# Optimization experiments

Hardware: AMD Instinct MI355X
Metric: run time of the kernel (lower is better)

Reference implementation:

```python
import jax, jax.numpy as jnp
import numpy as np

IN_FEATURES = 11008
OUT_FEATURES = 4096
TOPK = 5504            # in_features * topk_ratio (0.5)
RECALL_THRES = 0.9
N_CACHE = 64           # modeled steady-state cache size


def setup_inputs() -> dict:
    key = jax.random.key(0)
    k1, k2, k3, k4 = jax.random.split(key, 4)
    x = jax.random.normal(k1, (1, 1, IN_FEATURES), dtype=jnp.float32)
    weight = jax.random.normal(k2, (OUT_FEATURES, IN_FEATURES), dtype=jnp.float32) * 0.02
    bias = jax.random.normal(k3, (OUT_FEATURES,), dtype=jnp.float32) * 0.02
    cached_indices = jax.random.randint(k4, (N_CACHE, TOPK), 0, IN_FEATURES, dtype=jnp.int64)
    return {"x": x, "weight": weight, "bias": bias, "cached_indices": cached_indices}


def reference(x, weight, bias, cached_indices):
    # decode path: bsz == seq == 1
    xf = x.reshape(-1, IN_FEATURES)                       # [1, in]
    x_mean = jnp.abs(xf).mean(axis=0)                     # [in]
    # top-k neuron selection (argsort descending -> top_k)
    _, topk_idx = jax.lax.top_k(x_mean, TOPK)             # [topk]
    topk_mask = jnp.zeros((IN_FEATURES,), dtype=bool).at[topk_idx].set(True)
    # rebuild cached boolean masks from cached index sets
    cached_masks = (
        jnp.zeros((N_CACHE, IN_FEATURES), dtype=bool)
        .at[jnp.arange(N_CACHE)[:, None], cached_indices]
        .set(True)
    )
    # recall of each cached mask against current top-k mask
    intersection = jnp.sum(cached_masks & topk_mask[None, :], axis=1)  # [n_cache]
    recalls = intersection.astype(jnp.float32) / TOPK
    best_idx = jnp.argmax(recalls)
    best_recall = recalls[best_idx]
    # cache hit -> reuse cached indices; miss -> use fresh top-k indices
    idx = jnp.where(best_recall >= RECALL_THRES, cached_indices[best_idx], topk_idx)
    # gather sparse column slice, then small GEMM + bias
    w_slice = weight[:, idx]                               # [out, topk]
    out = xf[:, idx] @ w_slice.T + bias                    # [1, out]
    return out.reshape(1, 1, OUT_FEATURES)
```

## Files before the change

kernel.cpp:

```cpp
#include <hip/hip_runtime.h>
#include <stdint.h>

#define IN_F   11008
#define OUT_F  4096
#define TOPK_K 5504
#define NCACHE 64
#define MASK_WORDS 344
#define NCHUNK 11


__device__ __forceinline__ unsigned absbits(float v) {
    return __float_as_uint(v) & 0x7fffffffu;
}

__global__ __launch_bounds__(1024) void k_select(const float* __restrict__ x,
                                                 unsigned* __restrict__ maskbits_g,
                                                 unsigned* __restrict__ score_g) {
    __shared__ unsigned hist[16][256];
    __shared__ unsigned csum[256];
    __shared__ unsigned sh_T, sh_rem, sh_totEq;
    __shared__ unsigned waveEq[NCHUNK][16];
    __shared__ unsigned waveEqPre[NCHUNK][16];

    const int tid  = threadIdx.x;
    const int wv   = tid >> 6;
    const int lane = tid & 63;
    const int nk   = (tid < IN_F - 10 * 1024) ? NCHUNK : NCHUNK - 1;

    unsigned key[NCHUNK];
#pragma unroll
    for (int c = 0; c < NCHUNK; ++c) {
        key[c] = 0u;
        if (c < nk) key[c] = absbits(x[c * 1024 + tid]);
    }

    if (tid == 0) *score_g = 0;

    unsigned prefix = 0, maskHi = 0, remaining = TOPK_K;

    for (int pass = 3; pass >= 0; --pass) {
        const int sh = pass * 8;
        for (int b = tid; b < 16 * 256; b += 1024) ((unsigned*)hist)[b] = 0;
        __syncthreads();
#pragma unroll
        for (int c = 0; c < NCHUNK; ++c) {
            if (c < nk && (key[c] & maskHi) == prefix)
                atomicAdd(&hist[wv][(key[c] >> sh) & 255], 1u);
        }
        __syncthreads();
        if (tid < 256) {
            unsigned s = 0;
#pragma unroll
            for (int w = 0; w < 16; ++w) s += hist[w][tid];
            csum[tid] = s;
        }
        __syncthreads();
        if (wv == 0) {
            unsigned c0 = csum[4 * lane + 0], c1 = csum[4 * lane + 1];
            unsigned c2 = csum[4 * lane + 2], c3 = csum[4 * lane + 3];
            unsigned S = c0 + c1 + c2 + c3;
#pragma unroll
            for (int off = 1; off < 64; off <<= 1) {
                unsigned v = __shfl_down(S, off, 64);
                if (lane + off < 64) S += v;
            }
            unsigned Sn = __shfl_down(S, 1, 64);
            if (lane == 63) Sn = 0;
            unsigned t3 = Sn + c3;
            unsigned t2 = t3 + c2;
            unsigned t1 = t2 + c1;
            unsigned t0 = t1 + c0;
            unsigned rem = remaining;
            if (t3 >= rem && Sn < rem) { sh_T = prefix | ((unsigned)(4 * lane + 3) << sh); sh_rem = rem - Sn; }
            if (t2 >= rem && t3 < rem) { sh_T = prefix | ((unsigned)(4 * lane + 2) << sh); sh_rem = rem - t3; }
            if (t1 >= rem && t2 < rem) { sh_T = prefix | ((unsigned)(4 * lane + 1) << sh); sh_rem = rem - t2; }
            if (t0 >= rem && t1 < rem) { sh_T = prefix | ((unsigned)(4 * lane + 0) << sh); sh_rem = rem - t1; }
        }
        __syncthreads();
        prefix = sh_T;
        maskHi |= 0xffu << sh;
        remaining = sh_rem;
    }

    const unsigned T = prefix;
    const unsigned eqTake = remaining;

    unsigned gtm = 0, eqm = 0;
#pragma unroll
    for (int c = 0; c < NCHUNK; ++c) {
        if (c < nk) {
            if (key[c] > T)       gtm |= 1u << c;
            else if (key[c] == T) eqm |= 1u << c;
        }
    }
#pragma unroll
    for (int c = 0; c < NCHUNK; ++c) {
        unsigned long long bal = __ballot((eqm >> c) & 1u);
        if (lane == 0) waveEq[c][wv] = (unsigned)__popcll(bal);
    }
    __syncthreads();
    if (tid < 64) {
        unsigned s = 0;
        for (int p = lane; p < NCHUNK * 16; p += 64) s += waveEq[p >> 4][p & 15];
#pragma unroll
        for (int off = 32; off > 0; off >>= 1) s += __shfl_down(s, off, 64);
        if (lane == 0) sh_totEq = s;
    }
    __syncthreads();
    const bool fast = (sh_totEq == eqTake);
    if (!fast) {
        if (tid == 0) {
            unsigned run = 0;
            for (int c = 0; c < NCHUNK; ++c)
                for (int w = 0; w < 16; ++w) { waveEqPre[c][w] = run; run += waveEq[c][w]; }
        }
        __syncthreads();
    }
#pragma unroll
    for (int c = 0; c < NCHUNK; ++c) {
        bool eq = (eqm >> c) & 1u;
        bool take;
        if (fast) {
            take = (((gtm >> c) & 1u) != 0u) || eq;
        } else {
            unsigned long long balEq = __ballot(eq);
            unsigned rank = waveEqPre[c][wv] + (unsigned)__popcll(balEq & ((1ull << lane) - 1ull));
            take = (((gtm >> c) & 1u) != 0u) || (eq && rank < eqTake);
        }
        unsigned long long balT = __ballot(take);
        int w0 = c * 32 + wv * 2;
        if (w0 < MASK_WORDS && lane == 0) {
            maskbits_g[w0]     = (unsigned)balT;
            maskbits_g[w0 + 1] = (unsigned)(balT >> 32);
        }
    }
}

__global__ __launch_bounds__(256) void k_recall(const int* __restrict__ cached,
                                                const unsigned* __restrict__ maskbits_g,
                                                unsigned* __restrict__ score_g) {
    __shared__ unsigned rowbits[MASK_WORDS];
    __shared__ unsigned wsum[4];
    const int r = blockIdx.x;
    const int tid = threadIdx.x;
    for (int w = tid; w < MASK_WORDS; w += 256) rowbits[w] = 0;
    __syncthreads();
    const int4* ci4 = (const int4*)(cached + (size_t)r * TOPK_K);
    for (int t = tid; t < TOPK_K / 4; t += 256) {
        int4 v = ci4[t];
        atomicOr(&rowbits[v.x >> 5], 1u << (v.x & 31));
        atomicOr(&rowbits[v.y >> 5], 1u << (v.y & 31));
        atomicOr(&rowbits[v.z >> 5], 1u << (v.z & 31));
        atomicOr(&rowbits[v.w >> 5], 1u << (v.w & 31));
    }
    __syncthreads();
    unsigned cnt = 0;
    for (int w = tid; w < MASK_WORDS; w += 256) cnt += __popc(rowbits[w] & maskbits_g[w]);
    for (int off = 32; off > 0; off >>= 1) cnt += __shfl_down(cnt, off, 64);
    if ((tid & 63) == 0) wsum[tid >> 6] = cnt;
    __syncthreads();
    if (tid == 0) {
        unsigned tot = wsum[0] + wsum[1] + wsum[2] + wsum[3];
        atomicMax(score_g, (tot << 6) | (unsigned)(63 - r));
    }
}

#define ROWS_PER_BLOCK 16
#define GEMV_THREADS   512
__global__ __launch_bounds__(GEMV_THREADS) void k_gemv(const float* __restrict__ x,
                                                       const float* __restrict__ W,
                                                       const float* __restrict__ bias,
                                                       const unsigned* __restrict__ maskbits_g,
                                                       const unsigned* __restrict__ score_g,
                                                       const int* __restrict__ cached,
                                                       float* __restrict__ out) {
    __shared__ __align__(16) float xs[IN_F];
    const int tid = threadIdx.x;

    unsigned score = *score_g;
    unsigned inter = score >> 6;
    bool useCache = ((float)inter / (float)TOPK_K) >= 0.9f;

    if (useCache) {
        int best = 63 - (int)(score & 63u);
        for (int i = tid; i < IN_F; i += GEMV_THREADS) xs[i] = 0.f;
        __syncthreads();
        const int* ci = cached + (size_t)best * TOPK_K;
        for (int t = tid; t < TOPK_K; t += GEMV_THREADS) {
            int idx = ci[t];
            atomicAdd(&xs[idx], x[idx]);
        }
    } else {
        const float4* x4 = (const float4*)x;
        for (int j = tid; j < IN_F / 4; j += GEMV_THREADS) {
            float4 xv = x4[j];
            int base = j * 4;
            unsigned wbits = maskbits_g[base >> 5];
            int sh = base & 31;
            xs[base + 0] = xv.x * (float)((wbits >> (sh + 0)) & 1u);
            xs[base + 1] = xv.y * (float)((wbits >> (sh + 1)) & 1u);
            xs[base + 2] = xv.z * (float)((wbits >> (sh + 2)) & 1u);
            xs[base + 3] = xv.w * (float)((wbits >> (sh + 3)) & 1u);
        }
    }
    __syncthreads();

    const int wv   = tid >> 6;
    const int lane = tid & 63;
    const int row0 = blockIdx.x * ROWS_PER_BLOCK + wv * 2;
    const int row1 = row0 + 1;
    const float4* w0p = (const float4*)(W + (size_t)row0 * IN_F);
    const float4* w1p = (const float4*)(W + (size_t)row1 * IN_F);
    const float4* xs4 = (const float4*)xs;

    float acc0 = 0.f, acc1 = 0.f;
#pragma unroll 4
    for (int j = lane; j < IN_F / 4; j += 64) {
        float4 xv = xs4[j];
        float4 a  = w0p[j];
        float4 b  = w1p[j];
        acc0 += xv.x * a.x + xv.y * a.y + xv.z * a.z + xv.w * a.w;
        acc1 += xv.x * b.x + xv.y * b.y + xv.z * b.z + xv.w * b.w;
    }
    for (int off = 32; off > 0; off >>= 1) {
        acc0 += __shfl_down(acc0, off, 64);
        acc1 += __shfl_down(acc1, off, 64);
    }
    if (lane == 0) {
        out[row0] = acc0 + bias[row0];
        out[row1] = acc1 + bias[row1];
    }
}

extern "C" void kernel_launch(void* const* d_in, const int* in_sizes, int n_in,
                              void* d_out, int out_size, void* d_ws, size_t ws_size,
                              hipStream_t stream) {
    const float* x      = (const float*)d_in[0];
    const float* W      = (const float*)d_in[1];
    const float* bias   = (const float*)d_in[2];
    const int*   cached = (const int*)d_in[3];
    float* out = (float*)d_out;

    char* ws = (char*)d_ws;
    unsigned* maskbits = (unsigned*)(ws + 0);
    unsigned* score    = (unsigned*)(ws + 1408);

    k_select<<<1, 1024, 0, stream>>>(x, maskbits, score);
    k_recall<<<NCACHE, 256, 0, stream>>>(cached, maskbits, score);
    k_gemv<<<OUT_F / ROWS_PER_BLOCK, GEMV_THREADS, 0, stream>>>(x, W, bias, maskbits, score, cached, out);
}
```

Measured before the change: 280.1 us.

## Fuse select, recall and GEMV into one cooperative kernel with speculative GEMV

Merges the three launches into a single cooperative kernel of 256 blocks of 1024 threads, synchronised with grid.sync. While block 0 runs the top-k radix select, the other blocks touch their weight rows to warm the cache until a flag is raised. Each block then computes the GEMV speculatively with the fresh top-k mask while recall is still being evaluated. It redoes the GEMV with the cached index set only if the best recall passes the threshold. This removes launch gaps and overlaps selection with weight traffic, at the cost of two grid-wide barriers, a recompute on cache hits, and a single resident block per CU.

```diff
diff --git a/kernel.cpp b/kernel.cpp
--- a/kernel.cpp
+++ b/kernel.cpp
@@ -1,5 +1,8 @@
 #include <hip/hip_runtime.h>
+#include <hip/hip_cooperative_groups.h>
 #include <stdint.h>
+
+namespace cg = cooperative_groups;
 
 #define IN_F   11008
 #define OUT_F  4096
@@ -7,192 +10,196 @@
 #define NCACHE 64
 #define MASK_WORDS 344
 #define NCHUNK 11
+#define NBLK   256
+#define NTHR   1024
+#define ROWS_PER_BLOCK 16
 
 
 __device__ __forceinline__ unsigned absbits(float v) {
     return __float_as_uint(v) & 0x7fffffffu;
 }
 
-__global__ __launch_bounds__(1024) void k_select(const float* __restrict__ x,
-                                                 unsigned* __restrict__ maskbits_g,
-                                                 unsigned* __restrict__ score_g) {
+__global__ __launch_bounds__(NTHR) void k_fused(const float* __restrict__ x,
+                                                const float* __restrict__ W,
+                                                const float* __restrict__ bias,
+                                                const int* __restrict__ cached,
+                                                float* __restrict__ out,
+                                                unsigned* __restrict__ maskbits_g,
+                                                unsigned* __restrict__ score_g,
+                                                unsigned* __restrict__ flag_g) {
     __shared__ unsigned hist[16][256];
     __shared__ unsigned csum[256];
     __shared__ unsigned sh_T, sh_rem, sh_totEq;
     __shared__ unsigned waveEq[NCHUNK][16];
     __shared__ unsigned waveEqPre[NCHUNK][16];
+    __shared__ unsigned rowbits[MASK_WORDS];
+    __shared__ unsigned wsum[16];
+    __shared__ __align__(16) float xs[IN_F];
 
     const int tid  = threadIdx.x;
     const int wv   = tid >> 6;
     const int lane = tid & 63;
-    const int nk   = (tid < IN_F - 10 * 1024) ? NCHUNK : NCHUNK - 1;
-
-    unsigned key[NCHUNK];
-#pragma unroll
-    for (int c = 0; c < NCHUNK; ++c) {
-        key[c] = 0u;
-        if (c < nk) key[c] = absbits(x[c * 1024 + tid]);
-    }
-
-    if (tid == 0) *score_g = 0;
-
-    unsigned prefix = 0, maskHi = 0, remaining = TOPK_K;
-
-    for (int pass = 3; pass >= 0; --pass) {
-        const int sh = pass * 8;
-        for (int b = tid; b < 16 * 256; b += 1024) ((unsigned*)hist)[b] = 0;
-        __syncthreads();
-#pragma unroll
-        for (int c = 0; c < NCHUNK; ++c) {
-            if (c < nk && (key[c] & maskHi) == prefix)
-                atomicAdd(&hist[wv][(key[c] >> sh) & 255], 1u);
-        }
-        __syncthreads();
-        if (tid < 256) {
+    const int bid  = blockIdx.x;
+    cg::grid_group grid = cg::this_grid();
+
+    if (bid == 0) {
+        if (tid == 0) {
+            __hip_atomic_store(flag_g, 0u, __ATOMIC_RELAXED, __HIP_MEMORY_SCOPE_AGENT);
+            *score_g = 0u;
+        }
+        const int nk = (tid < IN_F - 10 * 1024) ? NCHUNK : NCHUNK - 1;
+
+        unsigned key[NCHUNK];
+#pragma unroll
+        for (int c = 0; c < NCHUNK; ++c) {
+            key[c] = 0u;
+            if (c < nk) key[c] = absbits(x[c * 1024 + tid]);
+        }
+
+        unsigned prefix = 0, maskHi = 0, remaining = TOPK_K;
+
+        for (int pass = 3; pass >= 0; --pass) {
+            const int sh = pass * 8;
+            for (int b = tid; b < 16 * 256; b += 1024) ((unsigned*)hist)[b] = 0;
+            __syncthreads();
+#pragma unroll
+            for (int c = 0; c < NCHUNK; ++c) {
+                if (c < nk && (key[c] & maskHi) == prefix)
+                    atomicAdd(&hist[wv][(key[c] >> sh) & 255], 1u);
+            }
+            __syncthreads();
+            if (tid < 256) {
+                unsigned s = 0;
+#pragma unroll
+                for (int w = 0; w < 16; ++w) s += hist[w][tid];
+                csum[tid] = s;
+            }
+            __syncthreads();
+            if (wv == 0) {
+                unsigned c0 = csum[4 * lane + 0], c1 = csum[4 * lane + 1];
+                unsigned c2 = csum[4 * lane + 2], c3 = csum[4 * lane + 3];
+                unsigned S = c0 + c1 + c2 + c3;
+#pragma unroll
+                for (int off = 1; off < 64; off <<= 1) {
+                    unsigned v = __shfl_down(S, off, 64);
+                    if (lane + off < 64) S += v;
+                }
+                unsigned Sn = __shfl_down(S, 1, 64);
+                if (lane == 63) Sn = 0;
+                unsigned t3 = Sn + c3;
+                unsigned t2 = t3 + c2;
+                unsigned t1 = t2 + c1;
+                unsigned t0 = t1 + c0;
+                unsigned rem = remaining;
+                if (t3 >= rem && Sn < rem) { sh_T = prefix | ((unsigned)(4 * lane + 3) << sh); sh_rem = rem - Sn; }
+                if (t2 >= rem && t3 < rem) { sh_T = prefix | ((unsigned)(4 * lane + 2) << sh); sh_rem = rem - t3; }
+                if (t1 >= rem && t2 < rem) { sh_T = prefix | ((unsigned)(4 * lane + 1) << sh); sh_rem = rem - t2; }
+                if (t0 >= rem && t1 < rem) { sh_T = prefix | ((unsigned)(4 * lane + 0) << sh); sh_rem = rem - t1; }
+            }
+            __syncthreads();
+            prefix = sh_T;
+            maskHi |= 0xffu << sh;
+            remaining = sh_rem;
+        }
+
+        const unsigned T = prefix;
+        const unsigned eqTake = remaining;
+
+        unsigned gtm = 0, eqm = 0;
+#pragma unroll
+        for (int c = 0; c < NCHUNK; ++c) {
+            if (c < nk) {
+                if (key[c] > T)       gtm |= 1u << c;
+                else if (key[c] == T) eqm |= 1u << c;
+            }
+        }
+#pragma unroll
+        for (int c = 0; c < NCHUNK; ++c) {
+            unsigned long long bal = __ballot((eqm >> c) & 1u);
+            if (lane == 0) waveEq[c][wv] = (unsigned)__popcll(bal);
+        }
+        __syncthreads();
+        if (tid < 64) {
             unsigned s = 0;
-#pragma unroll
-            for (int w = 0; w < 16; ++w) s += hist[w][tid];
-            csum[tid] = s;
-        }
-        __syncthreads();
-        if (wv == 0) {
-            unsigned c0 = csum[4 * lane + 0], c1 = csum[4 * lane + 1];
-            unsigned c2 = csum[4 * lane + 2], c3 = csum[4 * lane + 3];
-            unsigned S = c0 + c1 + c2 + c3;
-#pragma unroll
-            for (int off = 1; off < 64; off <<= 1) {
-                unsigned v = __shfl_down(S, off, 64);
-                if (lane + off < 64) S += v;
-            }
-            unsigned Sn = __shfl_down(S, 1, 64);
-            if (lane == 63) Sn = 0;
-            unsigned t3 = Sn + c3;
-            unsigned t2 = t3 + c2;
-            unsigned t1 = t2 + c1;
-            unsigned t0 = t1 + c0;
-            unsigned rem = remaining;
-            if (t3 >= rem && Sn < rem) { sh_T = prefix | ((unsigned)(4 * lane + 3) << sh); sh_rem = rem - Sn; }
-            if (t2 >= rem && t3 < rem) { sh_T = prefix | ((unsigned)(4 * lane + 2) << sh); sh_rem = rem - t3; }
-            if (t1 >= rem && t2 < rem) { sh_T = prefix | ((unsigned)(4 * lane + 1) << sh); sh_rem = rem - t2; }
-            if (t0 >= rem && t1 < rem) { sh_T = prefix | ((unsigned)(4 * lane + 0) << sh); sh_rem = rem - t1; }
-        }
-        __syncthreads();
-        prefix = sh_T;
-        maskHi |= 0xffu << sh;
-        remaining = sh_rem;
-    }
-
-    const unsigned T = prefix;
-    const unsigned eqTake = remaining;
-
-    unsigned gtm = 0, eqm = 0;
-#pragma unroll
-    for (int c = 0; c < NCHUNK; ++c) {
-        if (c < nk) {
-            if (key[c] > T)       gtm |= 1u << c;
-            else if (key[c] == T) eqm |= 1u << c;
-        }
-    }
-#pragma unroll
-    for (int c = 0; c < NCHUNK; ++c) {
-        unsigned long long bal = __ballot((eqm >> c) & 1u);
-        if (lane == 0) waveEq[c][wv] = (unsigned)__popcll(bal);
-    }
-    __syncthreads();
-    if (tid < 64) {
-        unsigned s = 0;
-        for (int p = lane; p < NCHUNK * 16; p += 64) s += waveEq[p >> 4][p & 15];
-#pragma unroll
-        for (int off = 32; off > 0; off >>= 1) s += __shfl_down(s, off, 64);
-        if (lane == 0) sh_totEq = s;
-    }
-    __syncthreads();
-    const bool fast = (sh_totEq == eqTake);
-    if (!fast) {
+            for (int p = lane; p < NCHUNK * 16; p += 64) s += waveEq[p >> 4][p & 15];
+#pragma unroll
+            for (int off = 32; off > 0; off >>= 1) s += __shfl_down(s, off, 64);
+            if (lane == 0) sh_totEq = s;
+        }
+        __syncthreads();
+        const bool fast = (sh_totEq == eqTake);
+        if (!fast) {
+            if (tid == 0) {
+                unsigned run = 0;
+                for (int c = 0; c < NCHUNK; ++c)
+                    for (int w = 0; w < 16; ++w) { waveEqPre[c][w] = run; run += waveEq[c][w]; }
+            }
+            __syncthreads();
+        }
+#pragma unroll
+        for (int c = 0; c < NCHUNK; ++c) {
+            bool eq = (eqm >> c) & 1u;
+            bool take;
+            if (fast) {
+                take = (((gtm >> c) & 1u) != 0u) || eq;
+            } else {
+                unsigned long long balEq = __ballot(eq);
+                unsigned rank = waveEqPre[c][wv] + (unsigned)__popcll(balEq & ((1ull << lane) - 1ull));
+                take = (((gtm >> c) & 1u) != 0u) || (eq && rank < eqTake);
+            }
+            unsigned long long balT = __ballot(take);
+            int w0 = c * 32 + wv * 2;
+            if (w0 < MASK_WORDS && lane == 0) {
+                maskbits_g[w0]     = (unsigned)balT;
+                maskbits_g[w0 + 1] = (unsigned)(balT >> 32);
+            }
+        }
+        __syncthreads();
+        if (tid == 0)
+            __hip_atomic_store(flag_g, 1u, __ATOMIC_RELAXED, __HIP_MEMORY_SCOPE_AGENT);
+    } else {
+        const float4* wp = (const float4*)(W + (size_t)bid * ROWS_PER_BLOCK * IN_F);
+        const int NCH = (ROWS_PER_BLOCK * IN_F / 4) / (2 * NTHR);
+        for (int c = 0; c < NCH; ++c) {
+            if (c >= 4 && __hip_atomic_load(flag_g, __ATOMIC_RELAXED, __HIP_MEMORY_SCOPE_AGENT) != 0u)
+                break;
+            float4 a = wp[c * 2 * NTHR + tid];
+            float4 b = wp[c * 2 * NTHR + NTHR + tid];
+            asm volatile("" :: "v"(a.x), "v"(a.y), "v"(a.z), "v"(a.w));
+            asm volatile("" :: "v"(b.x), "v"(b.y), "v"(b.z), "v"(b.w));
+        }
+    }
+
+    grid.sync();
+
+    if (bid < NCACHE) {
+        for (int w = tid; w < MASK_WORDS; w += NTHR) rowbits[w] = 0;
+        __syncthreads();
+        const int4* ci4 = (const int4*)(cached + (size_t)bid * TOPK_K);
+        for (int t = tid; t < TOPK_K / 4; t += NTHR) {
+            int4 v = ci4[t];
+            atomicOr(&rowbits[v.x >> 5], 1u << (v.x & 31));
+            atomicOr(&rowbits[v.y >> 5], 1u << (v.y & 31));
+            atomicOr(&rowbits[v.z >> 5], 1u << (v.z & 31));
+            atomicOr(&rowbits[v.w >> 5], 1u << (v.w & 31));
+        }
+        __syncthreads();
+        unsigned cnt = 0;
+        for (int w = tid; w < MASK_WORDS; w += NTHR) cnt += __popc(rowbits[w] & maskbits_g[w]);
+        for (int off = 32; off > 0; off >>= 1) cnt += __shfl_down(cnt, off, 64);
+        if (lane == 0) wsum[wv] = cnt;
+        __syncthreads();
         if (tid == 0) {
-            unsigned run = 0;
-            for (int c = 0; c < NCHUNK; ++c)
-                for (int w = 0; w < 16; ++w) { waveEqPre[c][w] = run; run += waveEq[c][w]; }
-        }
-        __syncthreads();
-    }
-#pragma unroll
-    for (int c = 0; c < NCHUNK; ++c) {
-        bool eq = (eqm >> c) & 1u;
-        bool take;
-        if (fast) {
-            take = (((gtm >> c) & 1u) != 0u) || eq;
-        } else {
-            unsigned long long balEq = __ballot(eq);
-            unsigned rank = waveEqPre[c][wv] + (unsigned)__popcll(balEq & ((1ull << lane) - 1ull));
-            take = (((gtm >> c) & 1u) != 0u) || (eq && rank < eqTake);
-        }
-        unsigned long long balT = __ballot(take);
-        int w0 = c * 32 + wv * 2;
-        if (w0 < MASK_WORDS && lane == 0) {
-            maskbits_g[w0]     = (unsigned)balT;
-            maskbits_g[w0 + 1] = (unsigned)(balT >> 32);
-        }
-    }
-}
-
-__global__ __launch_bounds__(256) void k_recall(const int* __restrict__ cached,
-                                                const unsigned* __restrict__ maskbits_g,
-                                                unsigned* __restrict__ score_g) {
-    __shared__ unsigned rowbits[MASK_WORDS];
-    __shared__ unsigned wsum[4];
-    const int r = blockIdx.x;
-    const int tid = threadIdx.x;
-    for (int w = tid; w < MASK_WORDS; w += 256) rowbits[w] = 0;
-    __syncthreads();
-    const int4* ci4 = (const int4*)(cached + (size_t)r * TOPK_K);
-    for (int t = tid; t < TOPK_K / 4; t += 256) {
-        int4 v = ci4[t];
-        atomicOr(&rowbits[v.x >> 5], 1u << (v.x & 31));
-        atomicOr(&rowbits[v.y >> 5], 1u << (v.y & 31));
-        atomicOr(&rowbits[v.z >> 5], 1u << (v.z & 31));
-        atomicOr(&rowbits[v.w >> 5], 1u << (v.w & 31));
-    }
-    __syncthreads();
-    unsigned cnt = 0;
-    for (int w = tid; w < MASK_WORDS; w += 256) cnt += __popc(rowbits[w] & maskbits_g[w]);
-    for (int off = 32; off > 0; off >>= 1) cnt += __shfl_down(cnt, off, 64);
-    if ((tid & 63) == 0) wsum[tid >> 6] = cnt;
-    __syncthreads();
-    if (tid == 0) {
-        unsigned tot = wsum[0] + wsum[1] + wsum[2] + wsum[3];
-        atomicMax(score_g, (tot << 6) | (unsigned)(63 - r));
-    }
-}
-
-#define ROWS_PER_BLOCK 16
-#define GEMV_THREADS   512
-__global__ __launch_bounds__(GEMV_THREADS) void k_gemv(const float* __restrict__ x,
-                                                       const float* __restrict__ W,
-                                                       const float* __restrict__ bias,
-                                                       const unsigned* __restrict__ maskbits_g,
-                                                       const unsigned* __restrict__ score_g,
-                                                       const int* __restrict__ cached,
-                                                       float* __restrict__ out) {
-    __shared__ __align__(16) float xs[IN_F];
-    const int tid = threadIdx.x;
-
-    unsigned score = *score_g;
-    unsigned inter = score >> 6;
-    bool useCache = ((float)inter / (float)TOPK_K) >= 0.9f;
-
-    if (useCache) {
-        int best = 63 - (int)(score & 63u);
-        for (int i = tid; i < IN_F; i += GEMV_THREADS) xs[i] = 0.f;
-        __syncthreads();
-        const int* ci = cached + (size_t)best * TOPK_K;
-        for (int t = tid; t < TOPK_K; t += GEMV_THREADS) {
-            int idx = ci[t];
-            atomicAdd(&xs[idx], x[idx]);
-        }
-    } else {
+            unsigned tot = 0;
+#pragma unroll
+            for (int w = 0; w < 16; ++w) tot += wsum[w];
+            atomicMax(score_g, (tot << 6) | (unsigned)(63 - bid));
+        }
+    }
+
+    {
         const float4* x4 = (const float4*)x;
-        for (int j = tid; j < IN_F / 4; j += GEMV_THREADS) {
+        for (int j = tid; j < IN_F / 4; j += NTHR) {
             float4 xv = x4[j];
             int base = j * 4;
             unsigned wbits = maskbits_g[base >> 5];
@@ -205,30 +212,45 @@
     }
     __syncthreads();
 
-    const int wv   = tid >> 6;
-    const int lane = tid & 63;
-    const int row0 = blockIdx.x * ROWS_PER_BLOCK + wv * 2;
-    const int row1 = row0 + 1;
-    const float4* w0p = (const float4*)(W + (size_t)row0 * IN_F);
-    const float4* w1p = (const float4*)(W + (size_t)row1 * IN_F);
-    const float4* xs4 = (const float4*)xs;
-
-    float acc0 = 0.f, acc1 = 0.f;
+    const int row = bid * ROWS_PER_BLOCK + wv;
+    const float4* wrow = (const float4*)(W + (size_t)row * IN_F);
+    const float4* xs4  = (const float4*)xs;
+
+    float acc = 0.f;
 #pragma unroll 4
     for (int j = lane; j < IN_F / 4; j += 64) {
+        float4 a  = wrow[j];
         float4 xv = xs4[j];
-        float4 a  = w0p[j];
-        float4 b  = w1p[j];
-        acc0 += xv.x * a.x + xv.y * a.y + xv.z * a.z + xv.w * a.w;
-        acc1 += xv.x * b.x + xv.y * b.y + xv.z * b.z + xv.w * b.w;
-    }
-    for (int off = 32; off > 0; off >>= 1) {
-        acc0 += __shfl_down(acc0, off, 64);
-        acc1 += __shfl_down(acc1, off, 64);
-    }
-    if (lane == 0) {
-        out[row0] = acc0 + bias[row0];
-        out[row1] = acc1 + bias[row1];
+        acc += xv.x * a.x + xv.y * a.y + xv.z * a.z + xv.w * a.w;
+    }
+    for (int off = 32; off > 0; off >>= 1) acc += __shfl_down(acc, off, 64);
+
+    grid.sync();
+
+    unsigned score = *score_g;
+    bool useCache = ((float)(score >> 6) / (float)TOPK_K) >= 0.9f;
+    if (!useCache) {
+        if (lane == 0) out[row] = acc + bias[row];
+    } else {
+        int best = 63 - (int)(score & 63u);
+        __syncthreads();
+        for (int i = tid; i < IN_F; i += NTHR) xs[i] = 0.f;
+        __syncthreads();
+        const int* ci = cached + (size_t)best * TOPK_K;
+        for (int t = tid; t < TOPK_K; t += NTHR) {
+            int idx = ci[t];
+            atomicAdd(&xs[idx], x[idx]);
+        }
+        __syncthreads();
+        float acc2 = 0.f;
+#pragma unroll 4
+        for (int j = lane; j < IN_F / 4; j += 64) {
+            float4 a  = wrow[j];
+            float4 xv = xs4[j];
+            acc2 += xv.x * a.x + xv.y * a.y + xv.z * a.z + xv.w * a.w;
+        }
+        for (int off = 32; off > 0; off >>= 1) acc2 += __shfl_down(acc2, off, 64);
+        if (lane == 0) out[row] = acc2 + bias[row];
     }
 }
 
@@ -244,8 +266,10 @@
     char* ws = (char*)d_ws;
     unsigned* maskbits = (unsigned*)(ws + 0);
     unsigned* score    = (unsigned*)(ws + 1408);
-
-    k_select<<<1, 1024, 0, stream>>>(x, maskbits, score);
-    k_recall<<<NCACHE, 256, 0, stream>>>(cached, maskbits, score);
-    k_gemv<<<OUT_F / ROWS_PER_BLOCK, GEMV_THREADS, 0, stream>>>(x, W, bias, maskbits, score, cached, out);
+    unsigned* flag     = (unsigned*)(ws + 1472);
+
+    void* args[] = { (void*)&x, (void*)&W, (void*)&bias, (void*)&cached,
+                     (void*)&out, (void*)&maskbits, (void*)&score, (void*)&flag };
+    hipLaunchCooperativeKernel((const void*)k_fused, dim3(NBLK), dim3(NTHR),
+                               args, 0, stream);
 }
```

After: 334.0 us. +19.3%, slower.

## Prefetch weights during top-k select and fuse recall with speculative GEMV

Applied to the files above, without the earlier changes.

The select kernel now runs extra blocks that stream weight rows into cache until block 0 raises a completion flag, so weight reads overlap the serial top-k pass. The recall and GEMV kernels are merged into one launch: GEMV blocks compute the fresh top-k result speculatively, then spin on a done counter bumped by the 64 recall blocks, and recompute with the cached index set only on a cache hit. This saves a launch and hides recall latency behind the GEMV. In exchange it relies on spin-waiting across blocks, which can deadlock if the recall blocks are not scheduled, and the prefetch only helps if weights stay resident in L2 or MALL.

```diff
diff --git a/kernel.cpp b/kernel.cpp
--- a/kernel.cpp
+++ b/kernel.cpp
@@ -7,15 +7,18 @@
 #define NCACHE 64
 #define MASK_WORDS 344
 #define NCHUNK 11
+#define ROWS_PER_BLOCK 16
+#define GEMV_THREADS   512
 
 
 __device__ __forceinline__ unsigned absbits(float v) {
     return __float_as_uint(v) & 0x7fffffffu;
 }
 
-__global__ __launch_bounds__(1024) void k_select(const float* __restrict__ x,
-                                                 unsigned* __restrict__ maskbits_g,
-                                                 unsigned* __restrict__ score_g) {
+__global__ __launch_bounds__(1024) void k_select_prefetch(const float* __restrict__ x,
+                                                          const float* __restrict__ W,
+                                                          unsigned* __restrict__ maskbits_g,
+                                                          unsigned* __restrict__ flag_g) {
     __shared__ unsigned hist[16][256];
     __shared__ unsigned csum[256];
     __shared__ unsigned sh_T, sh_rem, sh_totEq;
@@ -25,7 +28,23 @@
     const int tid  = threadIdx.x;
     const int wv   = tid >> 6;
     const int lane = tid & 63;
-    const int nk   = (tid < IN_F - 10 * 1024) ? NCHUNK : NCHUNK - 1;
+    const int bid  = blockIdx.x;
+
+    if (bid != 0) {
+        const float4* wp = (const float4*)(W + (size_t)bid * (ROWS_PER_BLOCK * IN_F));
+        const int NCH = (ROWS_PER_BLOCK * IN_F / 4) / (2 * 1024);
+        for (int c = 0; c < NCH; ++c) {
+            if (c >= 1 && __hip_atomic_load(flag_g, __ATOMIC_RELAXED, __HIP_MEMORY_SCOPE_AGENT) != 0u)
+                break;
+            float4 a = wp[c * 2048 + tid];
+            float4 b = wp[c * 2048 + 1024 + tid];
+            asm volatile("" :: "v"(a.x), "v"(a.y), "v"(a.z), "v"(a.w));
+            asm volatile("" :: "v"(b.x), "v"(b.y), "v"(b.z), "v"(b.w));
+        }
+        return;
+    }
+
+    const int nk = (tid < IN_F - 10 * 1024) ? NCHUNK : NCHUNK - 1;
 
     unsigned key[NCHUNK];
 #pragma unroll
@@ -33,8 +52,6 @@
         key[c] = 0u;
         if (c < nk) key[c] = absbits(x[c * 1024 + tid]);
     }
-
-    if (tid == 0) *score_g = 0;
 
     unsigned prefix = 0, maskHi = 0, remaining = TOPK_K;
 
@@ -134,80 +151,69 @@
             maskbits_g[w0 + 1] = (unsigned)(balT >> 32);
         }
     }
-}
-
-__global__ __launch_bounds__(256) void k_recall(const int* __restrict__ cached,
-                                                const unsigned* __restrict__ maskbits_g,
-                                                unsigned* __restrict__ score_g) {
+    __syncthreads();
+    if (tid == 0)
+        __hip_atomic_store(flag_g, 1u, __ATOMIC_RELAXED, __HIP_MEMORY_SCOPE_AGENT);
+}
+
+__global__ __launch_bounds__(GEMV_THREADS) void k_recall_gemv(const float* __restrict__ x,
+                                                              const float* __restrict__ W,
+                                                              const float* __restrict__ bias,
+                                                              const int* __restrict__ cached,
+                                                              const unsigned* __restrict__ maskbits_g,
+                                                              unsigned* __restrict__ score_g,
+                                                              unsigned* __restrict__ done_g,
+                                                              float* __restrict__ out) {
+    __shared__ __align__(16) float xs[IN_F];
     __shared__ unsigned rowbits[MASK_WORDS];
-    __shared__ unsigned wsum[4];
-    const int r = blockIdx.x;
-    const int tid = threadIdx.x;
-    for (int w = tid; w < MASK_WORDS; w += 256) rowbits[w] = 0;
-    __syncthreads();
-    const int4* ci4 = (const int4*)(cached + (size_t)r * TOPK_K);
-    for (int t = tid; t < TOPK_K / 4; t += 256) {
-        int4 v = ci4[t];
-        atomicOr(&rowbits[v.x >> 5], 1u << (v.x & 31));
-        atomicOr(&rowbits[v.y >> 5], 1u << (v.y & 31));
-        atomicOr(&rowbits[v.z >> 5], 1u << (v.z & 31));
-        atomicOr(&rowbits[v.w >> 5], 1u << (v.w & 31));
-    }
-    __syncthreads();
-    unsigned cnt = 0;
-    for (int w = tid; w < MASK_WORDS; w += 256) cnt += __popc(rowbits[w] & maskbits_g[w]);
-    for (int off = 32; off > 0; off >>= 1) cnt += __shfl_down(cnt, off, 64);
-    if ((tid & 63) == 0) wsum[tid >> 6] = cnt;
-    __syncthreads();
-    if (tid == 0) {
-        unsigned tot = wsum[0] + wsum[1] + wsum[2] + wsum[3];
-        atomicMax(score_g, (tot << 6) | (unsigned)(63 - r));
-    }
-}
-
-#define ROWS_PER_BLOCK 16
-#define GEMV_THREADS   512
-__global__ __launch_bounds__(GEMV_THREADS) void k_gemv(const float* __restrict__ x,
-                                                       const float* __restrict__ W,
-                                                       const float* __restrict__ bias,
-                                                       const unsigned* __restrict__ maskbits_g,
-                                                       const unsigned* __restrict__ score_g,
-                                                       const int* __restrict__ cached,
-                                                       float* __restrict__ out) {
-    __shared__ __align__(16) float xs[IN_F];
-    const int tid = threadIdx.x;
-
-    unsigned score = *score_g;
-    unsigned inter = score >> 6;
-    bool useCache = ((float)inter / (float)TOPK_K) >= 0.9f;
-
-    if (useCache) {
-        int best = 63 - (int)(score & 63u);
-        for (int i = tid; i < IN_F; i += GEMV_THREADS) xs[i] = 0.f;
-        __syncthreads();
-        const int* ci = cached + (size_t)best * TOPK_K;
-        for (int t = tid; t < TOPK_K; t += GEMV_THREADS) {
-            int idx = ci[t];
-            atomicAdd(&xs[idx], x[idx]);
-        }
-    } else {
-        const float4* x4 = (const float4*)x;
-        for (int j = tid; j < IN_F / 4; j += GEMV_THREADS) {
-            float4 xv = x4[j];
-            int base = j * 4;
-            unsigned wbits = maskbits_g[base >> 5];
-            int sh = base & 31;
-            xs[base + 0] = xv.x * (float)((wbits >> (sh + 0)) & 1u);
-            xs[base + 1] = xv.y * (float)((wbits >> (sh + 1)) & 1u);
-            xs[base + 2] = xv.z * (float)((wbits >> (sh + 2)) & 1u);
-            xs[base + 3] = xv.w * (float)((wbits >> (sh + 3)) & 1u);
-        }
-    }
-    __syncthreads();
-
+    __shared__ unsigned wsum[8];
+    const int tid  = threadIdx.x;
     const int wv   = tid >> 6;
     const int lane = tid & 63;
-    const int row0 = blockIdx.x * ROWS_PER_BLOCK + wv * 2;
+    const int bid  = blockIdx.x;
+
+    if (bid < NCACHE) {
+        for (int w = tid; w < MASK_WORDS; w += GEMV_THREADS) rowbits[w] = 0;
+        __syncthreads();
+        const int4* ci4 = (const int4*)(cached + (size_t)bid * TOPK_K);
+        for (int t = tid; t < TOPK_K / 4; t += GEMV_THREADS) {
+            int4 v = ci4[t];
+            atomicOr(&rowbits[v.x >> 5], 1u << (v.x & 31));
+            atomicOr(&rowbits[v.y >> 5], 1u << (v.y & 31));
+            atomicOr(&rowbits[v.z >> 5], 1u << (v.z & 31));
+            atomicOr(&rowbits[v.w >> 5], 1u << (v.w & 31));
+        }
+        __syncthreads();
+        unsigned cnt = 0;
+        for (int w = tid; w < MASK_WORDS; w += GEMV_THREADS) cnt += __popc(rowbits[w] & maskbits_g[w]);
+        for (int off = 32; off > 0; off >>= 1) cnt += __shfl_down(cnt, off, 64);
+        if (lane == 0) wsum[wv] = cnt;
+        __syncthreads();
+        if (tid == 0) {
+            unsigned tot = 0;
+#pragma unroll
+            for (int w = 0; w < 8; ++w) tot += wsum[w];
+            atomicMax(score_g, (tot << 6) | (unsigned)(63 - bid));
+            __hip_atomic_fetch_add(done_g, 1u, __ATOMIC_RELEASE, __HIP_MEMORY_SCOPE_AGENT);
+        }
+        return;
+    }
+
+    const int g = bid - NCACHE;
+    const float4* x4 = (const float4*)x;
+    for (int j = tid; j < IN_F / 4; j += GEMV_THREADS) {
+        float4 xv = x4[j];
+        int base = j * 4;
+        unsigned wbits = maskbits_g[base >> 5];
+        int sh = base & 31;
+        xs[base + 0] = xv.x * (float)((wbits >> (sh + 0)) & 1u);
+        xs[base + 1] = xv.y * (float)((wbits >> (sh + 1)) & 1u);
+        xs[base + 2] = xv.z * (float)((wbits >> (sh + 2)) & 1u);
+        xs[base + 3] = xv.w * (float)((wbits >> (sh + 3)) & 1u);
+    }
+    __syncthreads();
+
+    const int row0 = g * ROWS_PER_BLOCK + wv * 2;
     const int row1 = row0 + 1;
     const float4* w0p = (const float4*)(W + (size_t)row0 * IN_F);
     const float4* w1p = (const float4*)(W + (size_t)row1 * IN_F);
@@ -226,9 +232,48 @@
         acc0 += __shfl_down(acc0, off, 64);
         acc1 += __shfl_down(acc1, off, 64);
     }
-    if (lane == 0) {
-        out[row0] = acc0 + bias[row0];
-        out[row1] = acc1 + bias[row1];
+
+    if (tid == 0) {
+        while (__hip_atomic_load(done_g, __ATOMIC_ACQUIRE, __HIP_MEMORY_SCOPE_AGENT) < NCACHE)
+            __builtin_amdgcn_s_sleep(2);
+    }
+    __syncthreads();
+
+    unsigned score = *score_g;
+    bool useCache = ((float)(score >> 6) / (float)TOPK_K) >= 0.9f;
+    if (!useCache) {
+        if (lane == 0) {
+            out[row0] = acc0 + bias[row0];
+            out[row1] = acc1 + bias[row1];
+        }
+    } else {
+        int best = 63 - (int)(score & 63u);
+        __syncthreads();
+        for (int i = tid; i < IN_F; i += GEMV_THREADS) xs[i] = 0.f;
+        __syncthreads();
+        const int* ci = cached + (size_t)best * TOPK_K;
+        for (int t = tid; t < TOPK_K; t += GEMV_THREADS) {
+            int idx = ci[t];
+            atomicAdd(&xs[idx], x[idx]);
+        }
+        __syncthreads();
+        float a0 = 0.f, a1 = 0.f;
+#pragma unroll 4
+        for (int j = lane; j < IN_F / 4; j += 64) {
+            float4 xv = xs4[j];
+            float4 a  = w0p[j];
+            float4 b  = w1p[j];
+            a0 += xv.x * a.x + xv.y * a.y + xv.z * a.z + xv.w * a.w;
+            a1 += xv.x * b.x + xv.y * b.y + xv.z * b.z + xv.w * b.w;
+        }
+        for (int off = 32; off > 0; off >>= 1) {
+            a0 += __shfl_down(a0, off, 64);
+            a1 += __shfl_down(a1, off, 64);
+        }
+        if (lane == 0) {
+            out[row0] = a0 + bias[row0];
+            out[row1] = a1 + bias[row1];
+        }
     }
 }
 
@@ -243,9 +288,12 @@
 
     char* ws = (char*)d_ws;
     unsigned* maskbits = (unsigned*)(ws + 0);
-    unsigned* score    = (unsigned*)(ws + 1408);
-
-    k_select<<<1, 1024, 0, stream>>>(x, maskbits, score);
-    k_recall<<<NCACHE, 256, 0, stream>>>(cached, maskbits, score);
-    k_gemv<<<OUT_F / ROWS_PER_BLOCK, GEMV_THREADS, 0, stream>>>(x, W, bias, maskbits, score, cached, out);
-}
+    unsigned* score    = (unsigned*)(ws + 1472);
+    unsigned* flag     = (unsigned*)(ws + 1476);
+    unsigned* done     = (unsigned*)(ws + 1480);
+
+    hipMemsetAsync(ws + 1472, 0, 12, stream);
+    k_select_prefetch<<<256, 1024, 0, stream>>>(x, W, maskbits, flag);
+    k_recall_gemv<<<NCACHE + OUT_F / ROWS_PER_BLOCK, GEMV_THREADS, 0, stream>>>(
+        x, W, bias, cached, maskbits, score, done, out);
+}
```

After: 266.6 us. 4.8% less time.
